# Optimization experiments

Hardware: AMD Instinct MI355X
Metric: run time of the kernel (lower is better)

The kernel has to match this reference:

```python
import jax, jax.numpy as jnp
import numpy as np

NU, EU = 40000, 640000          # user-graph nodes / edges
B, T, NW, ET = 64, 16, 30, 60    # users, tweets/user, words/tweet, edges/tweet
NT = B * T * NW                  # 30720 tweet word-nodes
NTE = B * T * ET                 # 61440 tweet edges
NSEG_T = B * T                   # 1024 tweet segments


def gcn_conv(x, src, dst, W, b, N):
    """PyG GCNConv: x@W, add self loops, sym deg-normalize, scatter-add, +b."""
    x = x @ W
    loop = jnp.arange(N)
    s = jnp.concatenate([src, loop])
    d = jnp.concatenate([dst, loop])
    deg = jax.ops.segment_sum(jnp.ones_like(d, dtype=x.dtype), d, num_segments=N)
    dinv = jnp.where(deg > 0, jax.lax.rsqrt(deg), 0.0)
    norm = dinv[s] * dinv[d]                     # [E+N]
    out = jax.ops.segment_sum(x[s] * norm[:, None], d, num_segments=N)
    return out + b


def att_pool(x, seg, nseg, W1, b1, W2, b2):
    """AttentionalAggregation: gate_nn = Linear->Linear, segment softmax, weighted sum."""
    gate = (x @ W1 + b1) @ W2 + b2               # [N, C]
    m = jax.ops.segment_max(gate, seg, num_segments=nseg)
    e = jnp.exp(gate - m[seg])
    s = jax.ops.segment_sum(e, seg, num_segments=nseg)
    a = e / (s[seg] + 1e-16)
    return jax.ops.segment_sum(a * x, seg, num_segments=nseg)  # [nseg, C]


def gru_last(x_seq, W_ih, W_hh, b_ih, b_hh):
    """torch.nn.GRU, 1 layer; x_seq [B,T,C] -> final hidden [B,C]."""
    C = W_hh.shape[1]
    h0 = jnp.zeros((x_seq.shape[0], C), x_seq.dtype)
    def step(h, x):
        gi = x @ W_ih.T + b_ih
        gh = h @ W_hh.T + b_hh
        ir, iz, inn = jnp.split(gi, 3, axis=-1)
        hr, hz, hn = jnp.split(gh, 3, axis=-1)
        r = jax.nn.sigmoid(ir + hr)
        z = jax.nn.sigmoid(iz + hz)
        n = jnp.tanh(inn + r * hn)
        return (1.0 - z) * n + z * h, None
    hT, _ = jax.lax.scan(step, h0, jnp.swapaxes(x_seq, 0, 1))
    return hT


def setup_inputs():
    ks = jax.random.split(jax.random.key(0), 24)
    def rn(i, shape, s=1.0):
        return jax.random.normal(ks[i], shape, dtype=jnp.float32) * s
    z = lambda n_: jnp.zeros((n_,), jnp.float32)
    inp = {}
    inp["user_x"] = rn(0, (NU, 128))
    inp["user_feats"] = rn(1, (B, 32))
    inp["tweet_x"] = rn(2, (NT, 768))
    inp["Wu0"] = rn(3, (128, 128), 0.1); inp["bu0"] = z(128)
    inp["Wu1"] = rn(4, (128, 128), 0.1); inp["bu1"] = z(128)
    inp["Wgu1"] = rn(5, (128, 128), 0.1); inp["bgu1"] = z(128)
    inp["Wgu2"] = rn(6, (128, 128), 0.1); inp["bgu2"] = z(128)
    inp["Wt0"] = rn(7, (768, 256), 0.05); inp["bt0"] = z(256)
    inp["Wt1"] = rn(8, (256, 128), 0.1); inp["bt1"] = z(128)
    inp["Wgt1"] = rn(9, (128, 128), 0.1); inp["bgt1"] = z(128)
    inp["Wgt2"] = rn(10, (128, 128), 0.1); inp["bgt2"] = z(128)
    inp["W_ih"] = rn(11, (384, 128), 0.1); inp["b_ih"] = z(384)
    inp["W_hh"] = rn(12, (384, 128), 0.1); inp["b_hh"] = z(384)
    inp["Wd0"] = rn(13, (288, 256), 0.1); inp["bd0"] = z(256)
    inp["Wd1"] = rn(14, (256, 64), 0.1); inp["bd1"] = z(64)
    inp["Wp"] = rn(15, (64, 1), 0.1); inp["bp"] = z(1)
    inp["user_edge_index"] = jax.random.randint(ks[16], (2, EU), 0, NU)
    local = jax.random.randint(ks[17], (2, NTE), 0, NW)
    offs = jnp.repeat(jnp.arange(NSEG_T) * NW, ET)   # edges stay inside each tweet
    inp["tweet_edge_index"] = local + offs[None, :]
    inp["user_batch"] = jnp.arange(NU) // (NU // B)  # contiguous per-user segments (ptr)
    inp["tweet_batch"] = jnp.arange(NT) // NW        # contiguous per-tweet segments (ptr)
    return inp


def reference(user_x, user_feats, tweet_x,
              Wu0, bu0, Wu1, bu1, Wgu1, bgu1, Wgu2, bgu2,
              Wt0, bt0, Wt1, bt1, Wgt1, bgt1, Wgt2, bgt2,
              W_ih, b_ih, W_hh, b_hh,
              Wd0, bd0, Wd1, bd1, Wp, bp,
              user_edge_index, tweet_edge_index, user_batch, tweet_batch):
    h = jax.nn.relu(gcn_conv(user_x, user_edge_index[0], user_edge_index[1], Wu0, bu0, NU))
    h = jax.nn.relu(gcn_conv(h, user_edge_index[0], user_edge_index[1], Wu1, bu1, NU))
    user_pool = att_pool(h, user_batch, B, Wgu1, bgu1, Wgu2, bgu2)        # [B,128]
    g = jax.nn.relu(gcn_conv(tweet_x, tweet_edge_index[0], tweet_edge_index[1], Wt0, bt0, NT))
    g = jax.nn.relu(gcn_conv(g, tweet_edge_index[0], tweet_edge_index[1], Wt1, bt1, NT))
    tweet_pool = att_pool(g, tweet_batch, NSEG_T, Wgt1, bgt1, Wgt2, bgt2)  # [B*T,128]
    tweet_seq = tweet_pool.reshape(B, T, 128)
    tweet_h = gru_last(tweet_seq, W_ih, W_hh, b_ih, b_hh)                 # [B,128]
    # head
    full = jnp.concatenate([user_feats, user_pool, tweet_h], axis=1)      # [B,288]
    full = jax.nn.relu(full @ Wd0 + bd0)
    full = jax.nn.relu(full @ Wd1 + bd1)
    return jax.nn.sigmoid(full @ Wp + bp)                                 # [B,1]
```

## Files before the change

kernel.cpp:

```cpp
#include <hip/hip_runtime.h>
#include <hip/hip_bf16.h>

#define NU 40000
#define EU 640000
#define BB 64
#define TT 16
#define NW 30
#define NTNODES 30720
#define NTE 61440
#define NSEG_T 1024
#define NCHUNK 16
#define NBU 157
#define NBT 120

typedef __attribute__((ext_vector_type(8))) short bf16x8;
typedef __attribute__((ext_vector_type(4))) float f32x4;

__device__ __forceinline__ unsigned short f2bf(float x) {
    union { float f; unsigned u; } v; v.f = x;
    unsigned r = v.u + 0x7FFFu + ((v.u >> 16) & 1u);
    return (unsigned short)(r >> 16);
}
__device__ __forceinline__ float bf2f(unsigned short u) {
    union { unsigned u; float f; } v; v.u = (unsigned)u << 16; return v.f;
}
__device__ __forceinline__ void gld16(const unsigned short* g, unsigned short* l) {
    __builtin_amdgcn_global_load_lds(
        (const __attribute__((address_space(1))) void*)g,
        (__attribute__((address_space(3))) void*)l, 16, 0, 0);
}

__global__ void k_zeroint(int* __restrict__ p, int n) {
    int i = blockIdx.x * blockDim.x + threadIdx.x;
    if (i < n) p[i] = 0;
}

__global__ void k_hist2(const int* __restrict__ ue_dst, const int* __restrict__ te_dst,
                        int* __restrict__ hist_u, int* __restrict__ hist_t) {
    int i = blockIdx.x * blockDim.x + threadIdx.x;
    if (i < EU) atomicAdd(&hist_u[ue_dst[i]], 1);
    else if (i < EU + NTE) atomicAdd(&hist_t[te_dst[i - EU]], 1);
}

__global__ __launch_bounds__(256) void k_scan_a2(const int* __restrict__ hist_u,
                                                 int* __restrict__ bsum_u,
                                                 int* __restrict__ bsum_t) {
    __shared__ int red[256];
    int b = blockIdx.x, t = threadIdx.x;
    const int* h; int* bs; int n, lb;
    if (b < NBU) { h = hist_u;      bs = bsum_u; n = NU;      lb = b; }
    else         { h = hist_u + NU; bs = bsum_t; n = NTNODES; lb = b - NBU; }
    int i = lb * 256 + t;
    red[t] = (i < n) ? h[i] : 0;
    __syncthreads();
    for (int off = 128; off; off >>= 1) {
        if (t < off) red[t] += red[t + off];
        __syncthreads();
    }
    if (t == 0) bs[lb] = red[0];
}

__global__ __launch_bounds__(256) void k_scan_b2(int* __restrict__ bsum_u,
                                                 int* __restrict__ bsum_t) {
    __shared__ int s[256];
    int t = threadIdx.x;
    int* bs = blockIdx.x ? bsum_t : bsum_u;
    int nb  = blockIdx.x ? NBT : NBU;
    s[t] = (t < nb) ? bs[t] : 0;
    __syncthreads();
    for (int off = 1; off < 256; off <<= 1) {
        int v = (t >= off) ? s[t - off] : 0;
        __syncthreads();
        s[t] += v;
        __syncthreads();
    }
    if (t < nb) bs[t] = (t == 0) ? 0 : s[t - 1];
}

__global__ __launch_bounds__(256) void k_scan_c2(const int* __restrict__ hist_u,
                                                 const int* __restrict__ bsum_u,
                                                 const int* __restrict__ bsum_t,
                                                 int* __restrict__ ptr_u, int* __restrict__ fill_u,
                                                 int* __restrict__ ptr_t, int* __restrict__ fill_t,
                                                 float* __restrict__ dinv_u) {
    __shared__ int s[256];
    int b = blockIdx.x, t = threadIdx.x;
    const int *h, *bs; int *ptr, *fill; int n, lb; float* dv;
    if (b < NBU) { h = hist_u;      bs = bsum_u; ptr = ptr_u; fill = fill_u; n = NU;      lb = b;       dv = dinv_u; }
    else         { h = hist_u + NU; bs = bsum_t; ptr = ptr_t; fill = fill_t; n = NTNODES; lb = b - NBU; dv = dinv_u + NU; }
    int i = lb * 256 + t;
    int hv = (i < n) ? h[i] : 0;
    s[t] = hv;
    __syncthreads();
    for (int off = 1; off < 256; off <<= 1) {
        int v = (t >= off) ? s[t - off] : 0;
        __syncthreads();
        s[t] += v;
        __syncthreads();
    }
    if (i < n) {
        int excl = bs[lb] + s[t] - hv;
        ptr[i] = excl;
        fill[i] = excl;
        dv[i] = rsqrtf((float)hv + 1.0f);
        if (i == n - 1) ptr[n] = excl + hv;
    }
}

__global__ void k_place2(const int* __restrict__ ue_src, const int* __restrict__ ue_dst,
                         const int* __restrict__ te_src, const int* __restrict__ te_dst,
                         int* __restrict__ fill_u, int* __restrict__ esrc_u,
                         int* __restrict__ fill_t, int* __restrict__ esrc_t) {
    int e = blockIdx.x * blockDim.x + threadIdx.x;
    if (e < EU) {
        int pos = atomicAdd(&fill_u[ue_dst[e]], 1);
        esrc_u[pos] = ue_src[e];
    } else if (e < EU + NTE) {
        int e2 = e - EU;
        int pos = atomicAdd(&fill_t[te_dst[e2]], 1);
        esrc_t[pos] = te_src[e2];
    }
}

__global__ void k_transpose(const float* __restrict__ in, float* __restrict__ out,
                            int R, int K) {
    int idx = blockIdx.x * blockDim.x + threadIdx.x;
    if (idx >= R * K) return;
    int j = idx / K, k = idx - j * K;
    out[k * R + j] = in[idx];
}

__device__ __forceinline__ void pack_one(const float* __restrict__ W,
                                         unsigned short* __restrict__ out,
                                         int f, int K, int N, int trans) {
    int j = f & 7;
    int chunk = f >> 3;
    int c = chunk & 511;
    int panel = chunk >> 9;
    int KS = K >> 5;
    int ks = panel % KS;
    int bn = panel / KS;
    int n = bn * 128 + (c & 127);
    int k = ks * 32 + (c >> 7) * 8 + j;
    float v = trans ? W[(size_t)n * K + k] : W[(size_t)k * N + n];
    out[f] = f2bf(v);
}

__global__ void k_packall(const float* __restrict__ Wu0, const float* __restrict__ Wu1,
                          const float* __restrict__ Wgu1, const float* __restrict__ Wgu2,
                          const float* __restrict__ Wt0, const float* __restrict__ Wt1,
                          const float* __restrict__ Wgt1, const float* __restrict__ Wgt2,
                          const float* __restrict__ Wih,
                          unsigned short* __restrict__ pk) {
    int f = blockIdx.x * blockDim.x + threadIdx.x;
    if (f < 16384)        pack_one(Wu0,  pk + 0,      f,          128, 128, 0);
    else if (f < 32768)   pack_one(Wu1,  pk + 16384,  f - 16384,  128, 128, 0);
    else if (f < 49152)   pack_one(Wgu1, pk + 32768,  f - 32768,  128, 128, 0);
    else if (f < 65536)   pack_one(Wgu2, pk + 49152,  f - 49152,  128, 128, 0);
    else if (f < 262144)  pack_one(Wt0,  pk + 65536,  f - 65536,  768, 256, 0);
    else if (f < 294912)  pack_one(Wt1,  pk + 262144, f - 262144, 256, 128, 0);
    else if (f < 311296)  pack_one(Wgt1, pk + 294912, f - 294912, 128, 128, 0);
    else if (f < 327680)  pack_one(Wgt2, pk + 311296, f - 311296, 128, 128, 0);
    else if (f < 376832)  pack_one(Wih,  pk + 327680, f - 327680, 128, 384, 1);
}

template<bool AF32>
__global__ __launch_bounds__(256) void k_mgemm(const void* __restrict__ Araw,
                                               const unsigned short* __restrict__ Bpk,
                                               const float* __restrict__ bias,
                                               void* __restrict__ Craw,
                                               int M, int K, int N, int flags) {
    constexpr int AST = AF32 ? 260 : 256;
    __shared__ unsigned short Alds[8 * AST];
    __shared__ unsigned short Blds[8192];
    int tid = threadIdx.x, lane = tid & 63, w = tid >> 6;
    int bm = blockIdx.x, bn = blockIdx.y;
    int wr = (w >> 1) * 16, wc = (w & 1) * 64;
    int l15 = lane & 15, lk = lane >> 4;

    f32x4 acc[4];
#pragma unroll
    for (int n = 0; n < 4; ++n) acc[n] = (f32x4){0.f, 0.f, 0.f, 0.f};

    const unsigned short* Bpanel = Bpk + (size_t)bn * (K >> 5) * 4096;
    int KS64 = K >> 6;

    for (int ks = 0; ks < KS64; ++ks) {
        int k0 = ks * 64;
        {
            const unsigned short* bg = Bpanel + (size_t)ks * 8192;
#pragma unroll
            for (int q = 0; q < 4; ++q) {
                int off = (w * 4 + q) * 512;
                gld16(bg + off + lane * 8, &Blds[off]);
            }
        }
        if (AF32) {
            const float* A = (const float*)Araw;
#pragma unroll
            for (int p = 0; p < 2; ++p) {
                int f4 = p * 256 + tid;
                int row = f4 >> 4;
                int kq  = f4 & 15;
                float4 av = *(const float4*)(A + (size_t)(bm * 32 + row) * K + k0 + kq * 4);
                unsigned lo = (unsigned)f2bf(av.x) | ((unsigned)f2bf(av.y) << 16);
                unsigned hi = (unsigned)f2bf(av.z) | ((unsigned)f2bf(av.w) << 16);
                int off = (kq >> 1) * AST + row * 8 + (kq & 1) * 4;
                *(uint2*)&Alds[off] = make_uint2(lo, hi);
            }
        } else {
            const unsigned short* A = (const unsigned short*)Araw;
            int kblk = 2 * w + (lane >> 5);
            int row = lane & 31;
            gld16(A + (size_t)(bm * 32 + row) * K + k0 + kblk * 8,
                  &Alds[w * 512]);
        }
        __syncthreads();
#pragma unroll
        for (int h = 0; h < 2; ++h) {
            int kb = h * 4 + lk;
            bf16x8 a = *(const bf16x8*)&Alds[kb * AST + (wr + l15) * 8];
            bf16x8 b[4];
#pragma unroll
            for (int n = 0; n < 4; ++n)
                b[n] = *(const bf16x8*)&Blds[kb * 1024 + (wc + n * 16 + l15) * 8];
#pragma unroll
            for (int n = 0; n < 4; ++n)
                acc[n] = __builtin_amdgcn_mfma_f32_16x16x32_bf16(a, b[n], acc[n], 0, 0, 0);
        }
        __syncthreads();
    }

    int grow0 = bm * 32 + wr + lk * 4;
#pragma unroll
    for (int n = 0; n < 4; ++n) {
        int gcol = bn * 128 + wc + n * 16 + l15;
        float bv = (flags & 1) ? bias[gcol] : 0.f;
#pragma unroll
        for (int i = 0; i < 4; ++i) {
            int grow = grow0 + i;
            float v = acc[n][i] + bv;
            if (flags & 2) v = fmaxf(v, 0.f);
            if (flags & 4) ((float*)Craw)[(size_t)grow * N + gcol] = v;
            else ((unsigned short*)Craw)[(size_t)grow * N + gcol] = f2bf(v);
        }
    }
}

__global__ __launch_bounds__(256) void k_gatepair(const unsigned short* __restrict__ X,
                                                  const unsigned short* __restrict__ W1,
                                                  const float* __restrict__ b1,
                                                  const unsigned short* __restrict__ W2,
                                                  const float* __restrict__ b2,
                                                  unsigned short* __restrict__ outp, int M) {
    __shared__ unsigned short Ax[16 * 512];
    __shared__ unsigned short Wl[8192];
    int tid = threadIdx.x, lane = tid & 63, w = tid >> 6;
    int bm = blockIdx.x;
    int wr = (w >> 1) * 32, wc = (w & 1) * 64;
    int l15 = lane & 15, lk = lane >> 4;

#pragma unroll
    for (int q = 0; q < 4; ++q) {
        int pl = w * 4 + q;
        gld16(X + (size_t)(bm * 64 + lane) * 128 + pl * 8, &Ax[pl * 512]);
    }

    f32x4 acc[2][4];
#pragma unroll
    for (int m = 0; m < 2; ++m)
#pragma unroll
        for (int n = 0; n < 4; ++n) acc[m][n] = (f32x4){0.f, 0.f, 0.f, 0.f};

    for (int ks = 0; ks < 2; ++ks) {
        const unsigned short* wp = W1 + ks * 8192;
#pragma unroll
        for (int q = 0; q < 4; ++q) {
            int off = (w * 4 + q) * 512;
            gld16(wp + off + lane * 8, &Wl[off]);
        }
        __syncthreads();
#pragma unroll
        for (int h = 0; h < 2; ++h) {
            int kb = h * 4 + lk;
            bf16x8 a[2], b[4];
#pragma unroll
            for (int m = 0; m < 2; ++m)
                a[m] = *(const bf16x8*)&Ax[(ks * 8 + kb) * 512 + (wr + m * 16 + l15) * 8];
#pragma unroll
            for (int n = 0; n < 4; ++n)
                b[n] = *(const bf16x8*)&Wl[kb * 1024 + (wc + n * 16 + l15) * 8];
#pragma unroll
            for (int m = 0; m < 2; ++m)
#pragma unroll
                for (int n = 0; n < 4; ++n)
                    acc[m][n] = __builtin_amdgcn_mfma_f32_16x16x32_bf16(a[m], b[n], acc[m][n], 0, 0, 0);
        }
        __syncthreads();
    }

#pragma unroll
    for (int m = 0; m < 2; ++m)
#pragma unroll
        for (int n = 0; n < 4; ++n) {
            int col = wc + n * 16 + l15;
            float bv = b1[col];
#pragma unroll
            for (int i = 0; i < 4; ++i) {
                int row = wr + m * 16 + lk * 4 + i;
                float v = acc[m][n][i] + bv;
                Ax[(col >> 3) * 512 + row * 8 + (col & 7)] = f2bf(v);
            }
        }
    __syncthreads();

#pragma unroll
    for (int m = 0; m < 2; ++m)
#pragma unroll
        for (int n = 0; n < 4; ++n) acc[m][n] = (f32x4){0.f, 0.f, 0.f, 0.f};
    for (int ks = 0; ks < 2; ++ks) {
        const unsigned short* wp = W2 + ks * 8192;
#pragma unroll
        for (int q = 0; q < 4; ++q) {
            int off = (w * 4 + q) * 512;
            gld16(wp + off + lane * 8, &Wl[off]);
        }
        __syncthreads();
#pragma unroll
        for (int h = 0; h < 2; ++h) {
            int kb = h * 4 + lk;
            bf16x8 a[2], b[4];
#pragma unroll
            for (int m = 0; m < 2; ++m)
                a[m] = *(const bf16x8*)&Ax[(ks * 8 + kb) * 512 + (wr + m * 16 + l15) * 8];
#pragma unroll
            for (int n = 0; n < 4; ++n)
                b[n] = *(const bf16x8*)&Wl[kb * 1024 + (wc + n * 16 + l15) * 8];
#pragma unroll
            for (int m = 0; m < 2; ++m)
#pragma unroll
                for (int n = 0; n < 4; ++n)
                    acc[m][n] = __builtin_amdgcn_mfma_f32_16x16x32_bf16(a[m], b[n], acc[m][n], 0, 0, 0);
        }
        __syncthreads();
    }

#pragma unroll
    for (int m = 0; m < 2; ++m)
#pragma unroll
        for (int n = 0; n < 4; ++n) {
            int col = wc + n * 16 + l15;
            float bv = b2[col];
#pragma unroll
            for (int i = 0; i < 4; ++i) {
                int row = bm * 64 + wr + m * 16 + lk * 4 + i;
                float v = acc[m][n][i] + bv;
                outp[(size_t)row * 128 + col] = f2bf(v);
            }
        }
}

__global__ __launch_bounds__(256) void k_gagg(const unsigned short* __restrict__ y,
                                              const int* __restrict__ ptr,
                                              const int* __restrict__ esrc,
                                              const float* __restrict__ dinv,
                                              const float* __restrict__ bias,
                                              unsigned short* __restrict__ ob, int N, int nch) {
    int idx = blockIdx.x * 4 + (threadIdx.x >> 6);
    if (idx >= N * nch) return;
    int v = idx / nch, ch = idx - v * nch;
    int C = nch << 7;
    int lane = threadIdx.x & 63;
    int c0 = (ch << 7) + lane * 2;
    float dv = dinv[v];
    unsigned yv = *(const unsigned*)(y + (size_t)v * C + c0);
    float a0 = dv * dv * bf2f((unsigned short)yv);
    float a1 = dv * dv * bf2f((unsigned short)(yv >> 16));
    int e = ptr[v], e1 = ptr[v + 1];
    for (; e + 3 < e1; e += 4) {
        int s0 = esrc[e], s1 = esrc[e + 1], s2 = esrc[e + 2], s3 = esrc[e + 3];
        float cc0 = dv * dinv[s0], cc1 = dv * dinv[s1];
        float cc2 = dv * dinv[s2], cc3 = dv * dinv[s3];
        unsigned w0 = *(const unsigned*)(y + (size_t)s0 * C + c0);
        unsigned w1 = *(const unsigned*)(y + (size_t)s1 * C + c0);
        unsigned w2 = *(const unsigned*)(y + (size_t)s2 * C + c0);
        unsigned w3 = *(const unsigned*)(y + (size_t)s3 * C + c0);
        a0 += cc0 * bf2f((unsigned short)w0) + cc1 * bf2f((unsigned short)w1)
            + cc2 * bf2f((unsigned short)w2) + cc3 * bf2f((unsigned short)w3);
        a1 += cc0 * bf2f((unsigned short)(w0 >> 16)) + cc1 * bf2f((unsigned short)(w1 >> 16))
            + cc2 * bf2f((unsigned short)(w2 >> 16)) + cc3 * bf2f((unsigned short)(w3 >> 16));
    }
    for (; e < e1; ++e) {
        int s0 = esrc[e];
        float cc0 = dv * dinv[s0];
        unsigned w0 = *(const unsigned*)(y + (size_t)s0 * C + c0);
        a0 += cc0 * bf2f((unsigned short)w0);
        a1 += cc0 * bf2f((unsigned short)(w0 >> 16));
    }
    a0 = fmaxf(a0 + bias[c0], 0.f);
    a1 = fmaxf(a1 + bias[c0 + 1], 0.f);
    *(unsigned*)(ob + (size_t)v * C + c0) = (unsigned)f2bf(a0) | ((unsigned)f2bf(a1) << 16);
}

__global__ __launch_bounds__(128) void k_attpool(const unsigned short* __restrict__ x,
                                                 const unsigned short* __restrict__ gate,
                                                 unsigned short* __restrict__ outb, int S) {
    int seg = blockIdx.x;
    int c = threadIdx.x;
    size_t base = (size_t)seg * S * 128 + c;
    float m = -1e30f;
    for (int n = 0; n < S; ++n) m = fmaxf(m, bf2f(gate[base + (size_t)n * 128]));
    float se = 0.f, acc = 0.f;
    for (int n = 0; n < S; ++n) {
        float g = bf2f(gate[base + (size_t)n * 128]);
        float e = expf(g - m);
        se += e;
        acc += e * bf2f(x[base + (size_t)n * 128]);
    }
    outb[(size_t)seg * 128 + c] = f2bf(acc / (se + 1e-16f));
}

__global__ __launch_bounds__(256) void k_pool_pmax(const unsigned short* __restrict__ gate,
                                                   float* __restrict__ pmax, int S) {
    int seg = blockIdx.x, ch = blockIdx.y;
    int c = threadIdx.x & 127, j = threadIdx.x >> 7;
    int csz = (S + NCHUNK - 1) / NCHUNK;
    int n0 = ch * csz, n1 = min(S, n0 + csz);
    size_t base = (size_t)seg * S * 128 + c;
    float m = -1e30f;
    for (int n = n0 + j; n < n1; n += 2)
        m = fmaxf(m, bf2f(gate[base + (size_t)n * 128]));
    __shared__ float red[2][128];
    red[j][c] = m;
    __syncthreads();
    if (j == 0)
        pmax[((size_t)seg * NCHUNK + ch) * 128 + c] = fmaxf(red[0][c], red[1][c]);
}

__global__ __launch_bounds__(256) void k_pool_psum(const unsigned short* __restrict__ x,
                                                   const unsigned short* __restrict__ gate,
                                                   const float* __restrict__ pmax,
                                                   float* __restrict__ pse,
                                                   float* __restrict__ pacc, int S) {
    int seg = blockIdx.x, ch = blockIdx.y;
    int c = threadIdx.x & 127, j = threadIdx.x >> 7;
    int csz = (S + NCHUNK - 1) / NCHUNK;
    int n0 = ch * csz, n1 = min(S, n0 + csz);
    size_t base = (size_t)seg * S * 128 + c;
    float m = -1e30f;
#pragma unroll
    for (int ch2 = 0; ch2 < NCHUNK; ++ch2)
        m = fmaxf(m, pmax[((size_t)seg * NCHUNK + ch2) * 128 + c]);
    float se = 0.f, acc = 0.f;
    for (int n = n0 + j; n < n1; n += 2) {
        float g = bf2f(gate[base + (size_t)n * 128]);
        float e = expf(g - m);
        se += e;
        acc += e * bf2f(x[base + (size_t)n * 128]);
    }
    __shared__ float rs[2][128], ra[2][128];
    rs[j][c] = se; ra[j][c] = acc;
    __syncthreads();
    if (j == 0) {
        size_t o = ((size_t)seg * NCHUNK + ch) * 128 + c;
        pse[o]  = rs[0][c] + rs[1][c];
        pacc[o] = ra[0][c] + ra[1][c];
    }
}

__global__ __launch_bounds__(128) void k_pool_final(const float* __restrict__ pse,
                                                    const float* __restrict__ pacc,
                                                    float* __restrict__ out) {
    int seg = blockIdx.x, c = threadIdx.x;
    float se = 0.f, acc = 0.f;
    for (int ch = 0; ch < NCHUNK; ++ch) {
        size_t o = ((size_t)seg * NCHUNK + ch) * 128 + c;
        se += pse[o];
        acc += pacc[o];
    }
    out[(size_t)seg * 128 + c] = acc / (se + 1e-16f);
}

__global__ __launch_bounds__(768) void k_gru_rec(const float* __restrict__ gi,
                                                 const float* __restrict__ whhT,
                                                 const float* __restrict__ bhh,
                                                 float* __restrict__ hT) {
    __shared__ float hs[128];
    __shared__ float ph[768];
    int b = blockIdx.x, t = threadIdx.x;
    int half = (t >= 384) ? 1 : 0;
    int j = t - half * 384;
    float w[64];
#pragma unroll
    for (int i = 0; i < 64; ++i)
        w[i] = whhT[(half * 64 + i) * 384 + j];
    float chr = 0.f, chz = 0.f, chn = 0.f;
    if (t < 128) {
        hs[t] = 0.f;
        chr = bhh[t]; chz = bhh[128 + t]; chn = bhh[256 + t];
    }
    __syncthreads();
    for (int step = 0; step < TT; ++step) {
        float a0 = 0.f, a1 = 0.f, a2 = 0.f, a3 = 0.f;
        const float* hbase = hs + half * 64;
#pragma unroll
        for (int i = 0; i < 64; i += 4) {
            float4 hv = *(const float4*)(hbase + i);
            a0 += hv.x * w[i + 0];
            a1 += hv.y * w[i + 1];
            a2 += hv.z * w[i + 2];
            a3 += hv.w * w[i + 3];
        }
        ph[t] = (a0 + a1) + (a2 + a3);
        __syncthreads();
        float hnew = 0.f;
        if (t < 128) {
            const float* girow = gi + ((size_t)b * TT + step) * 384;
            float hr = ph[t] + ph[t + 384] + chr;
            float hz = ph[128 + t] + ph[512 + t] + chz;
            float hn = ph[256 + t] + ph[640 + t] + chn;
            float ir = girow[t], iz = girow[128 + t], in = girow[256 + t];
            float r = 1.f / (1.f + expf(-(ir + hr)));
            float z = 1.f / (1.f + expf(-(iz + hz)));
            float n = tanhf(in + r * hn);
            hnew = (1.f - z) * n + z * hs[t];
        }
        __syncthreads();
        if (t < 128) hs[t] = hnew;
        __syncthreads();
    }
    if (t < 128) hT[(size_t)b * 128 + t] = hs[t];
}

__global__ __launch_bounds__(256) void k_head(const float* __restrict__ uf,
                                              const float* __restrict__ up,
                                              const float* __restrict__ th,
                                              const float* __restrict__ Wd0, const float* __restrict__ bd0,
                                              const float* __restrict__ Wd1, const float* __restrict__ bd1,
                                              const float* __restrict__ Wp, const float* __restrict__ bp,
                                              float* __restrict__ out) {
    __shared__ float in0[288], l1[256], l2[64];
    int b = blockIdx.x, t = threadIdx.x;
    if (t < 32) in0[t] = uf[b * 32 + t];
    else if (t < 160) in0[t] = up[b * 128 + (t - 32)];
    if (t < 128) in0[160 + t] = th[b * 128 + t];
    __syncthreads();
    float acc = bd0[t];
    for (int k = 0; k < 288; ++k) acc += in0[k] * Wd0[k * 256 + t];
    l1[t] = fmaxf(acc, 0.f);
    __syncthreads();
    if (t < 64) {
        float a2 = bd1[t];
        for (int k = 0; k < 256; ++k) a2 += l1[k] * Wd1[k * 64 + t];
        l2[t] = fmaxf(a2, 0.f);
    }
    __syncthreads();
    if (t < 64) {
        float p = l2[t] * Wp[t];
        for (int off = 32; off; off >>= 1) p += __shfl_down(p, off, 64);
        if (t == 0) out[b] = 1.f / (1.f + expf(-(p + bp[0])));
    }
}

extern "C" void kernel_launch(void* const* d_in, const int* in_sizes, int n_in,
                              void* d_out, int out_size, void* d_ws, size_t ws_size,
                              hipStream_t stream) {
    const float* user_x     = (const float*)d_in[0];
    const float* user_feats = (const float*)d_in[1];
    const float* tweet_x    = (const float*)d_in[2];
    const float* Wu0 = (const float*)d_in[3];  const float* bu0 = (const float*)d_in[4];
    const float* Wu1 = (const float*)d_in[5];  const float* bu1 = (const float*)d_in[6];
    const float* Wgu1 = (const float*)d_in[7]; const float* bgu1 = (const float*)d_in[8];
    const float* Wgu2 = (const float*)d_in[9]; const float* bgu2 = (const float*)d_in[10];
    const float* Wt0 = (const float*)d_in[11]; const float* bt0 = (const float*)d_in[12];
    const float* Wt1 = (const float*)d_in[13]; const float* bt1 = (const float*)d_in[14];
    const float* Wgt1 = (const float*)d_in[15]; const float* bgt1 = (const float*)d_in[16];
    const float* Wgt2 = (const float*)d_in[17]; const float* bgt2 = (const float*)d_in[18];
    const float* W_ih = (const float*)d_in[19]; const float* b_ih = (const float*)d_in[20];
    const float* W_hh = (const float*)d_in[21]; const float* b_hh = (const float*)d_in[22];
    const float* Wd0 = (const float*)d_in[23]; const float* bd0 = (const float*)d_in[24];
    const float* Wd1 = (const float*)d_in[25]; const float* bd1 = (const float*)d_in[26];
    const float* Wp  = (const float*)d_in[27]; const float* bp  = (const float*)d_in[28];
    const int* ue = (const int*)d_in[29];
    const int* te = (const int*)d_in[30];
    const int* ue_src = ue, *ue_dst = ue + EU;
    const int* te_src = te, *te_dst = te + NTE;

    float* ws = (float*)d_ws;
    size_t o = 0;
    float* dinv_u = ws + o;     o += NU;
    float* dinv_t = ws + o;     o += NTNODES;
    float* user_pool = ws + o;  o += (size_t)BB * 128;
    float* tweet_h = ws + o;    o += (size_t)BB * 128;
    float* whhT = ws + o;       o += 128 * 384;
    float* gi = ws + o;         o += (size_t)NSEG_T * 384;
    float* pmax = ws + o;       o += 131072;
    float* pse = ws + o;        o += 131072;
    float* pacc = ws + o;       o += 131072;
    int* iw = (int*)(ws + o);
    int* hist_u = iw;
    int* hist_t = iw + NU;
    int* ptr_u  = iw + NU + NTNODES;
    int* fill_u = ptr_u + NU + 1;
    int* esrc_u = fill_u + NU;
    int* ptr_t  = esrc_u + EU;
    int* fill_t = ptr_t + NTNODES + 1;
    int* esrc_t = fill_t + NTNODES;
    int* bsum_u = esrc_t + NTE;
    int* bsum_t = bsum_u + 256;
    unsigned short* pk = (unsigned short*)(((uintptr_t)(bsum_t + 256) + 15) & ~(uintptr_t)15);
    unsigned short* pWu0  = pk;
    unsigned short* pWu1  = pWu0  + 16384;
    unsigned short* pWgu1 = pWu1  + 16384;
    unsigned short* pWgu2 = pWgu1 + 16384;
    unsigned short* pWt0  = pWgu2 + 16384;
    unsigned short* pWt1  = pWt0  + 196608;
    unsigned short* pWgt1 = pWt1  + 32768;
    unsigned short* pWgt2 = pWgt1 + 16384;
    unsigned short* pWih  = pWgt2 + 16384;
    unsigned short* arena = (unsigned short*)(((uintptr_t)(pWih + 49152) + 15) & ~(uintptr_t)15);
    const size_t SLOT = (size_t)NTNODES * 256;
    unsigned short* P0 = arena;
    unsigned short* P1 = P0 + SLOT;
    unsigned short* P2 = P1 + SLOT;
    unsigned short* P3 = P2 + SLOT;
    unsigned short* tpool_bf = P3 + SLOT;
    float* out = (float*)d_out;

    dim3 b256(256);
    const int GMU = NU / 32;
    const int GMT = NTNODES / 32;
    const float* NB = nullptr;

    hipLaunchKernelGGL(k_packall, dim3((376832 + 255) / 256), b256, 0, stream,
                       Wu0, Wu1, Wgu1, Wgu2, Wt0, Wt1, Wgt1, Wgt2, W_ih, pk);
    hipLaunchKernelGGL(k_transpose, dim3((384 * 128 + 255) / 256), b256, 0, stream,
                       W_hh, whhT, 384, 128);

    hipLaunchKernelGGL(k_zeroint, dim3((NU + NTNODES + 255) / 256), b256, 0, stream,
                       hist_u, NU + NTNODES);
    hipLaunchKernelGGL(k_hist2, dim3((EU + NTE + 255) / 256), b256, 0, stream,
                       ue_dst, te_dst, hist_u, hist_t);
    hipLaunchKernelGGL(k_scan_a2, dim3(NBU + NBT), b256, 0, stream, hist_u, bsum_u, bsum_t);
    hipLaunchKernelGGL(k_scan_b2, dim3(2), b256, 0, stream, bsum_u, bsum_t);
    hipLaunchKernelGGL(k_scan_c2, dim3(NBU + NBT), b256, 0, stream,
                       hist_u, bsum_u, bsum_t, ptr_u, fill_u, ptr_t, fill_t, dinv_u);
    hipLaunchKernelGGL(k_place2, dim3((EU + NTE + 255) / 256), b256, 0, stream,
                       ue_src, ue_dst, te_src, te_dst, fill_u, esrc_u, fill_t, esrc_t);

    hipLaunchKernelGGL(HIP_KERNEL_NAME(k_mgemm<true>), dim3(GMT, 2), b256, 0, stream,
                       (const void*)tweet_x, pWt0, NB, (void*)P0, NTNODES, 768, 256, 0);
    hipLaunchKernelGGL(k_gagg, dim3((NTNODES * 2 + 3) / 4), b256, 0, stream,
                       P0, ptr_t, esrc_t, dinv_t, bt0, P1, NTNODES, 2);

    hipLaunchKernelGGL(HIP_KERNEL_NAME(k_mgemm<true>), dim3(GMU, 1), b256, 0, stream,
                       (const void*)user_x, pWu0, NB, (void*)P3, NU, 128, 128, 0);
    hipLaunchKernelGGL(k_gagg, dim3((NU + 3) / 4), b256, 0, stream,
                       P3, ptr_u, esrc_u, dinv_u, bu0, P0, NU, 1);
    hipLaunchKernelGGL(HIP_KERNEL_NAME(k_mgemm<false>), dim3(GMU, 1), b256, 0, stream,
                       (const void*)P0, pWu1, NB, (void*)P2, NU, 128, 128, 0);
    hipLaunchKernelGGL(k_gagg, dim3((NU + 3) / 4), b256, 0, stream,
                       P2, ptr_u, esrc_u, dinv_u, bu1, P3, NU, 1);
    hipLaunchKernelGGL(k_gatepair, dim3(NU / 64), b256, 0, stream,
                       P3, pWgu1, bgu1, pWgu2, bgu2, P0, NU);
    hipLaunchKernelGGL(k_pool_pmax, dim3(BB, NCHUNK), b256, 0, stream, P0, pmax, NU / BB);
    hipLaunchKernelGGL(k_pool_psum, dim3(BB, NCHUNK), b256, 0, stream,
                       P3, P0, pmax, pse, pacc, NU / BB);
    hipLaunchKernelGGL(k_pool_final, dim3(BB), dim3(128), 0, stream, pse, pacc, user_pool);

    hipLaunchKernelGGL(HIP_KERNEL_NAME(k_mgemm<false>), dim3(GMT, 1), b256, 0, stream,
                       (const void*)P1, pWt1, NB, (void*)P2, NTNODES, 256, 128, 0);
    hipLaunchKernelGGL(k_gagg, dim3((NTNODES + 3) / 4), b256, 0, stream,
                       P2, ptr_t, esrc_t, dinv_t, bt1, P3, NTNODES, 1);
    hipLaunchKernelGGL(k_gatepair, dim3(NTNODES / 64), b256, 0, stream,
                       P3, pWgt1, bgt1, pWgt2, bgt2, P1, NTNODES);
    hipLaunchKernelGGL(k_attpool, dim3(NSEG_T), dim3(128), 0, stream,
                       P3, P1, tpool_bf, NW);

    hipLaunchKernelGGL(HIP_KERNEL_NAME(k_mgemm<false>), dim3(NSEG_T / 32, 3), b256, 0, stream,
                       (const void*)tpool_bf, pWih, b_ih, (void*)gi, NSEG_T, 128, 384, 5);
    hipLaunchKernelGGL(k_gru_rec, dim3(BB), dim3(768), 0, stream,
                       gi, whhT, b_hh, tweet_h);

    hipLaunchKernelGGL(k_head, dim3(BB), b256, 0, stream,
                       user_feats, user_pool, tweet_h,
                       Wd0, bd0, Wd1, bd1, Wp, bp, out);
}
```

Measured before the change: 345.1 us.

## Use 128x128 MFMA GEMM tiles and pre-convert fp32 inputs to bf16

Replaces the 32-row GEMM tile with a 128x128 tile where each wave computes a 64x64 block using a 4x4 grid of MFMA accumulators. This raises operand reuse per LDS load and cuts redundant B-panel reads across blocks. A separate conversion kernel now casts user_x and tweet_x to bf16 up front, so every GEMM takes bf16 inputs through async global-to-LDS loads. In exchange, the conversion adds an extra full pass over the large tweet_x input plus a write of its bf16 copy, and the larger tiles yield far fewer blocks for the small GEMMs (for example, 8 blocks on the 1024-row input-projection GEMM).

```diff
diff --git a/kernel.cpp b/kernel.cpp
--- a/kernel.cpp
+++ b/kernel.cpp
@@ -128,6 +128,25 @@
     if (idx >= R * K) return;
     int j = idx / K, k = idx - j * K;
     out[k * R + j] = in[idx];
+}
+
+#define NUX ((long)NU * 128)
+#define NTX ((long)NTNODES * 768)
+__global__ void k_cvt2(const float* __restrict__ ux, const float* __restrict__ tx,
+                       unsigned short* __restrict__ xu, unsigned short* __restrict__ xt) {
+    long i = ((long)blockIdx.x * blockDim.x + threadIdx.x) * 8;
+    const float* src; unsigned short* dst; long j;
+    if (i < NUX) { src = ux; dst = xu; j = i; }
+    else if (i < NUX + NTX) { src = tx; dst = xt; j = i - NUX; }
+    else return;
+    float4 a = *(const float4*)(src + j);
+    float4 b = *(const float4*)(src + j + 4);
+    uint4 r;
+    r.x = (unsigned)f2bf(a.x) | ((unsigned)f2bf(a.y) << 16);
+    r.y = (unsigned)f2bf(a.z) | ((unsigned)f2bf(a.w) << 16);
+    r.z = (unsigned)f2bf(b.x) | ((unsigned)f2bf(b.y) << 16);
+    r.w = (unsigned)f2bf(b.z) | ((unsigned)f2bf(b.w) << 16);
+    *(uint4*)(dst + j) = r;
 }
 
 __device__ __forceinline__ void pack_one(const float* __restrict__ W,
@@ -164,85 +183,79 @@
     else if (f < 376832)  pack_one(Wih,  pk + 327680, f - 327680, 128, 384, 1);
 }
 
-template<bool AF32>
-__global__ __launch_bounds__(256) void k_mgemm(const void* __restrict__ Araw,
-                                               const unsigned short* __restrict__ Bpk,
-                                               const float* __restrict__ bias,
-                                               void* __restrict__ Craw,
-                                               int M, int K, int N, int flags) {
-    constexpr int AST = AF32 ? 260 : 256;
-    __shared__ unsigned short Alds[8 * AST];
-    __shared__ unsigned short Blds[8192];
+__global__ __launch_bounds__(256) void k_mgemm128(const unsigned short* __restrict__ A,
+                                                  const unsigned short* __restrict__ Bpk,
+                                                  const float* __restrict__ bias,
+                                                  void* __restrict__ Craw,
+                                                  int M, int K, int N, int flags) {
+    __shared__ unsigned short Alds[4096];
+    __shared__ unsigned short Blds[4096];
     int tid = threadIdx.x, lane = tid & 63, w = tid >> 6;
     int bm = blockIdx.x, bn = blockIdx.y;
-    int wr = (w >> 1) * 16, wc = (w & 1) * 64;
+    int wr = (w >> 1) * 64, wc = (w & 1) * 64;
     int l15 = lane & 15, lk = lane >> 4;
 
-    f32x4 acc[4];
-#pragma unroll
-    for (int n = 0; n < 4; ++n) acc[n] = (f32x4){0.f, 0.f, 0.f, 0.f};
-
-    const unsigned short* Bpanel = Bpk + (size_t)bn * (K >> 5) * 4096;
-    int KS64 = K >> 6;
-
-    for (int ks = 0; ks < KS64; ++ks) {
-        int k0 = ks * 64;
+    f32x4 acc[4][4];
+#pragma unroll
+    for (int m = 0; m < 4; ++m)
+#pragma unroll
+        for (int n = 0; n < 4; ++n) acc[m][n] = (f32x4){0.f, 0.f, 0.f, 0.f};
+
+    int KS = K >> 5;
+    const unsigned short* Bpanel = Bpk + (size_t)bn * KS * 4096;
+
+    for (int ks = 0; ks < KS; ++ks) {
+        int k0 = ks * 32;
         {
-            const unsigned short* bg = Bpanel + (size_t)ks * 8192;
-#pragma unroll
-            for (int q = 0; q < 4; ++q) {
-                int off = (w * 4 + q) * 512;
-                gld16(bg + off + lane * 8, &Blds[off]);
+            const unsigned short* bg = Bpanel + (size_t)ks * 4096;
+#pragma unroll
+            for (int q = 0; q < 2; ++q) {
+                int i = w * 2 + q;
+                gld16(bg + i * 512 + lane * 8, &Blds[i * 512]);
             }
         }
-        if (AF32) {
-            const float* A = (const float*)Araw;
-#pragma unroll
-            for (int p = 0; p < 2; ++p) {
-                int f4 = p * 256 + tid;
-                int row = f4 >> 4;
-                int kq  = f4 & 15;
-                float4 av = *(const float4*)(A + (size_t)(bm * 32 + row) * K + k0 + kq * 4);
-                unsigned lo = (unsigned)f2bf(av.x) | ((unsigned)f2bf(av.y) << 16);
-                unsigned hi = (unsigned)f2bf(av.z) | ((unsigned)f2bf(av.w) << 16);
-                int off = (kq >> 1) * AST + row * 8 + (kq & 1) * 4;
-                *(uint2*)&Alds[off] = make_uint2(lo, hi);
+#pragma unroll
+        for (int q = 0; q < 2; ++q) {
+            int i = w * 2 + q;
+            int kblk = i >> 1, half = i & 1;
+            int rg = bm * 128 + half * 64 + lane;
+            rg = rg < M ? rg : M - 1;
+            gld16(A + (size_t)rg * K + k0 + kblk * 8,
+                  &Alds[kblk * 1024 + half * 512]);
+        }
+        __syncthreads();
+        bf16x8 a[4], b[4];
+#pragma unroll
+        for (int m = 0; m < 4; ++m)
+            a[m] = *(const bf16x8*)&Alds[lk * 1024 + (wr + m * 16 + l15) * 8];
+#pragma unroll
+        for (int n = 0; n < 4; ++n)
+            b[n] = *(const bf16x8*)&Blds[lk * 1024 + (wc + n * 16 + l15) * 8];
+#pragma unroll
+        for (int m = 0; m < 4; ++m)
+#pragma unroll
+            for (int n = 0; n < 4; ++n)
+                acc[m][n] = __builtin_amdgcn_mfma_f32_16x16x32_bf16(a[m], b[n], acc[m][n], 0, 0, 0);
+        __syncthreads();
+    }
+
+#pragma unroll
+    for (int m = 0; m < 4; ++m) {
+        int grow0 = bm * 128 + wr + m * 16 + lk * 4;
+#pragma unroll
+        for (int n = 0; n < 4; ++n) {
+            int gcol = bn * 128 + wc + n * 16 + l15;
+            float bv = (flags & 1) ? bias[gcol] : 0.f;
+#pragma unroll
+            for (int i = 0; i < 4; ++i) {
+                int grow = grow0 + i;
+                if (grow < M) {
+                    float v = acc[m][n][i] + bv;
+                    if (flags & 2) v = fmaxf(v, 0.f);
+                    if (flags & 4) ((float*)Craw)[(size_t)grow * N + gcol] = v;
+                    else ((unsigned short*)Craw)[(size_t)grow * N + gcol] = f2bf(v);
+                }
             }
-        } else {
-            const unsigned short* A = (const unsigned short*)Araw;
-            int kblk = 2 * w + (lane >> 5);
-            int row = lane & 31;
-            gld16(A + (size_t)(bm * 32 + row) * K + k0 + kblk * 8,
-                  &Alds[w * 512]);
-        }
-        __syncthreads();
-#pragma unroll
-        for (int h = 0; h < 2; ++h) {
-            int kb = h * 4 + lk;
-            bf16x8 a = *(const bf16x8*)&Alds[kb * AST + (wr + l15) * 8];
-            bf16x8 b[4];
-#pragma unroll
-            for (int n = 0; n < 4; ++n)
-                b[n] = *(const bf16x8*)&Blds[kb * 1024 + (wc + n * 16 + l15) * 8];
-#pragma unroll
-            for (int n = 0; n < 4; ++n)
-                acc[n] = __builtin_amdgcn_mfma_f32_16x16x32_bf16(a, b[n], acc[n], 0, 0, 0);
-        }
-        __syncthreads();
-    }
-
-    int grow0 = bm * 32 + wr + lk * 4;
-#pragma unroll
-    for (int n = 0; n < 4; ++n) {
-        int gcol = bn * 128 + wc + n * 16 + l15;
-        float bv = (flags & 1) ? bias[gcol] : 0.f;
-#pragma unroll
-        for (int i = 0; i < 4; ++i) {
-            int grow = grow0 + i;
-            float v = acc[n][i] + bv;
-            if (flags & 2) v = fmaxf(v, 0.f);
-            if (flags & 4) ((float*)Craw)[(size_t)grow * N + gcol] = v;
-            else ((unsigned short*)Craw)[(size_t)grow * N + gcol] = f2bf(v);
         }
     }
 }
@@ -625,17 +638,21 @@
     unsigned short* P2 = P1 + SLOT;
     unsigned short* P3 = P2 + SLOT;
     unsigned short* tpool_bf = P3 + SLOT;
+    unsigned short* xt = P1;
+    unsigned short* xu = tpool_bf + 131072;
     float* out = (float*)d_out;
 
     dim3 b256(256);
-    const int GMU = NU / 32;
-    const int GMT = NTNODES / 32;
+    const int GMU = (NU + 127) / 128;
+    const int GMT = NTNODES / 128;
     const float* NB = nullptr;
 
     hipLaunchKernelGGL(k_packall, dim3((376832 + 255) / 256), b256, 0, stream,
                        Wu0, Wu1, Wgu1, Wgu2, Wt0, Wt1, Wgt1, Wgt2, W_ih, pk);
     hipLaunchKernelGGL(k_transpose, dim3((384 * 128 + 255) / 256), b256, 0, stream,
                        W_hh, whhT, 384, 128);
+    hipLaunchKernelGGL(k_cvt2, dim3((int)((NUX + NTX) / 8 / 256 + 1)), b256, 0, stream,
+                       user_x, tweet_x, xu, xt);
 
     hipLaunchKernelGGL(k_zeroint, dim3((NU + NTNODES + 255) / 256), b256, 0, stream,
                        hist_u, NU + NTNODES);
@@ -648,17 +665,17 @@
     hipLaunchKernelGGL(k_place2, dim3((EU + NTE + 255) / 256), b256, 0, stream,
                        ue_src, ue_dst, te_src, te_dst, fill_u, esrc_u, fill_t, esrc_t);
 
-    hipLaunchKernelGGL(HIP_KERNEL_NAME(k_mgemm<true>), dim3(GMT, 2), b256, 0, stream,
-                       (const void*)tweet_x, pWt0, NB, (void*)P0, NTNODES, 768, 256, 0);
+    hipLaunchKernelGGL(k_mgemm128, dim3(GMT, 2), b256, 0, stream,
+                       xt, pWt0, NB, (void*)P0, NTNODES, 768, 256, 0);
     hipLaunchKernelGGL(k_gagg, dim3((NTNODES * 2 + 3) / 4), b256, 0, stream,
                        P0, ptr_t, esrc_t, dinv_t, bt0, P1, NTNODES, 2);
 
-    hipLaunchKernelGGL(HIP_KERNEL_NAME(k_mgemm<true>), dim3(GMU, 1), b256, 0, stream,
-                       (const void*)user_x, pWu0, NB, (void*)P3, NU, 128, 128, 0);
+    hipLaunchKernelGGL(k_mgemm128, dim3(GMU, 1), b256, 0, stream,
+                       xu, pWu0, NB, (void*)P3, NU, 128, 128, 0);
     hipLaunchKernelGGL(k_gagg, dim3((NU + 3) / 4), b256, 0, stream,
                        P3, ptr_u, esrc_u, dinv_u, bu0, P0, NU, 1);
-    hipLaunchKernelGGL(HIP_KERNEL_NAME(k_mgemm<false>), dim3(GMU, 1), b256, 0, stream,
-                       (const void*)P0, pWu1, NB, (void*)P2, NU, 128, 128, 0);
+    hipLaunchKernelGGL(k_mgemm128, dim3(GMU, 1), b256, 0, stream,
+                       P0, pWu1, NB, (void*)P2, NU, 128, 128, 0);
     hipLaunchKernelGGL(k_gagg, dim3((NU + 3) / 4), b256, 0, stream,
                        P2, ptr_u, esrc_u, dinv_u, bu1, P3, NU, 1);
     hipLaunchKernelGGL(k_gatepair, dim3(NU / 64), b256, 0, stream,
@@ -668,8 +685,8 @@
                        P3, P0, pmax, pse, pacc, NU / BB);
     hipLaunchKernelGGL(k_pool_final, dim3(BB), dim3(128), 0, stream, pse, pacc, user_pool);
 
-    hipLaunchKernelGGL(HIP_KERNEL_NAME(k_mgemm<false>), dim3(GMT, 1), b256, 0, stream,
-                       (const void*)P1, pWt1, NB, (void*)P2, NTNODES, 256, 128, 0);
+    hipLaunchKernelGGL(k_mgemm128, dim3(GMT, 1), b256, 0, stream,
+                       P1, pWt1, NB, (void*)P2, NTNODES, 256, 128, 0);
     hipLaunchKernelGGL(k_gagg, dim3((NTNODES + 3) / 4), b256, 0, stream,
                        P2, ptr_t, esrc_t, dinv_t, bt1, P3, NTNODES, 1);
     hipLaunchKernelGGL(k_gatepair, dim3(NTNODES / 64), b256, 0, stream,
@@ -677,8 +694,8 @@
     hipLaunchKernelGGL(k_attpool, dim3(NSEG_T), dim3(128), 0, stream,
                        P3, P1, tpool_bf, NW);
 
-    hipLaunchKernelGGL(HIP_KERNEL_NAME(k_mgemm<false>), dim3(NSEG_T / 32, 3), b256, 0, stream,
-                       (const void*)tpool_bf, pWih, b_ih, (void*)gi, NSEG_T, 128, 384, 5);
+    hipLaunchKernelGGL(k_mgemm128, dim3(NSEG_T / 128, 3), b256, 0, stream,
+                       tpool_bf, pWih, b_ih, (void*)gi, NSEG_T, 128, 384, 5);
     hipLaunchKernelGGL(k_gru_rec, dim3(BB), dim3(768), 0, stream,
                        gi, whhT, b_hh, tweet_h);
 
```

Result: slower. 410.9 us (+19.1%).

## Fold GCN source-side degree scaling into GEMM epilogue and merge transpose into pack

Applied to the files above, without the earlier changes.

Each GCN layer's feature GEMM now scales its output rows by dinv, so the aggregation kernel sums neighbor rows without gathering dinv per edge, applying the destination dinv once at the end. This removes per-edge dinv loads and multiplies from the gather-heavy aggregation. The W_hh transpose is folded into the weight-packing kernel, saving one launch. Rows are scaled before bf16 rounding, which slightly changes numerics.

```diff
diff --git a/kernel.cpp b/kernel.cpp
--- a/kernel.cpp
+++ b/kernel.cpp
@@ -122,14 +122,6 @@
     }
 }
 
-__global__ void k_transpose(const float* __restrict__ in, float* __restrict__ out,
-                            int R, int K) {
-    int idx = blockIdx.x * blockDim.x + threadIdx.x;
-    if (idx >= R * K) return;
-    int j = idx / K, k = idx - j * K;
-    out[k * R + j] = in[idx];
-}
-
 __device__ __forceinline__ void pack_one(const float* __restrict__ W,
                                          unsigned short* __restrict__ out,
                                          int f, int K, int N, int trans) {
@@ -151,6 +143,7 @@
                           const float* __restrict__ Wt0, const float* __restrict__ Wt1,
                           const float* __restrict__ Wgt1, const float* __restrict__ Wgt2,
                           const float* __restrict__ Wih,
+                          const float* __restrict__ Whh, float* __restrict__ whhT,
                           unsigned short* __restrict__ pk) {
     int f = blockIdx.x * blockDim.x + threadIdx.x;
     if (f < 16384)        pack_one(Wu0,  pk + 0,      f,          128, 128, 0);
@@ -162,12 +155,18 @@
     else if (f < 311296)  pack_one(Wgt1, pk + 294912, f - 294912, 128, 128, 0);
     else if (f < 327680)  pack_one(Wgt2, pk + 311296, f - 311296, 128, 128, 0);
     else if (f < 376832)  pack_one(Wih,  pk + 327680, f - 327680, 128, 384, 1);
+    else if (f < 425984) {
+        int j2 = f - 376832;
+        int r = j2 >> 7, k2 = j2 & 127;
+        whhT[k2 * 384 + r] = Whh[j2];
+    }
 }
 
 template<bool AF32>
 __global__ __launch_bounds__(256) void k_mgemm(const void* __restrict__ Araw,
                                                const unsigned short* __restrict__ Bpk,
                                                const float* __restrict__ bias,
+                                               const float* __restrict__ dscale,
                                                void* __restrict__ Craw,
                                                int M, int K, int N, int flags) {
     constexpr int AST = AF32 ? 260 : 256;
@@ -233,13 +232,14 @@
 
     int grow0 = bm * 32 + wr + lk * 4;
 #pragma unroll
-    for (int n = 0; n < 4; ++n) {
-        int gcol = bn * 128 + wc + n * 16 + l15;
-        float bv = (flags & 1) ? bias[gcol] : 0.f;
-#pragma unroll
-        for (int i = 0; i < 4; ++i) {
-            int grow = grow0 + i;
-            float v = acc[n][i] + bv;
+    for (int i = 0; i < 4; ++i) {
+        int grow = grow0 + i;
+        float ds = dscale ? dscale[grow] : 1.f;
+#pragma unroll
+        for (int n = 0; n < 4; ++n) {
+            int gcol = bn * 128 + wc + n * 16 + l15;
+            float v = acc[n][i] * ds;
+            if (flags & 1) v += bias[gcol];
             if (flags & 2) v = fmaxf(v, 0.f);
             if (flags & 4) ((float*)Craw)[(size_t)grow * N + gcol] = v;
             else ((unsigned short*)Craw)[(size_t)grow * N + gcol] = f2bf(v);
@@ -372,33 +372,30 @@
     int C = nch << 7;
     int lane = threadIdx.x & 63;
     int c0 = (ch << 7) + lane * 2;
-    float dv = dinv[v];
     unsigned yv = *(const unsigned*)(y + (size_t)v * C + c0);
-    float a0 = dv * dv * bf2f((unsigned short)yv);
-    float a1 = dv * dv * bf2f((unsigned short)(yv >> 16));
+    float a0 = bf2f((unsigned short)yv);
+    float a1 = bf2f((unsigned short)(yv >> 16));
     int e = ptr[v], e1 = ptr[v + 1];
     for (; e + 3 < e1; e += 4) {
         int s0 = esrc[e], s1 = esrc[e + 1], s2 = esrc[e + 2], s3 = esrc[e + 3];
-        float cc0 = dv * dinv[s0], cc1 = dv * dinv[s1];
-        float cc2 = dv * dinv[s2], cc3 = dv * dinv[s3];
         unsigned w0 = *(const unsigned*)(y + (size_t)s0 * C + c0);
         unsigned w1 = *(const unsigned*)(y + (size_t)s1 * C + c0);
         unsigned w2 = *(const unsigned*)(y + (size_t)s2 * C + c0);
         unsigned w3 = *(const unsigned*)(y + (size_t)s3 * C + c0);
-        a0 += cc0 * bf2f((unsigned short)w0) + cc1 * bf2f((unsigned short)w1)
-            + cc2 * bf2f((unsigned short)w2) + cc3 * bf2f((unsigned short)w3);
-        a1 += cc0 * bf2f((unsigned short)(w0 >> 16)) + cc1 * bf2f((unsigned short)(w1 >> 16))
-            + cc2 * bf2f((unsigned short)(w2 >> 16)) + cc3 * bf2f((unsigned short)(w3 >> 16));
+        a0 += bf2f((unsigned short)w0) + bf2f((unsigned short)w1)
+            + bf2f((unsigned short)w2) + bf2f((unsigned short)w3);
+        a1 += bf2f((unsigned short)(w0 >> 16)) + bf2f((unsigned short)(w1 >> 16))
+            + bf2f((unsigned short)(w2 >> 16)) + bf2f((unsigned short)(w3 >> 16));
     }
     for (; e < e1; ++e) {
         int s0 = esrc[e];
-        float cc0 = dv * dinv[s0];
         unsigned w0 = *(const unsigned*)(y + (size_t)s0 * C + c0);
-        a0 += cc0 * bf2f((unsigned short)w0);
-        a1 += cc0 * bf2f((unsigned short)(w0 >> 16));
-    }
-    a0 = fmaxf(a0 + bias[c0], 0.f);
-    a1 = fmaxf(a1 + bias[c0 + 1], 0.f);
+        a0 += bf2f((unsigned short)w0);
+        a1 += bf2f((unsigned short)(w0 >> 16));
+    }
+    float dv = dinv[v];
+    a0 = fmaxf(dv * a0 + bias[c0], 0.f);
+    a1 = fmaxf(dv * a1 + bias[c0 + 1], 0.f);
     *(unsigned*)(ob + (size_t)v * C + c0) = (unsigned)f2bf(a0) | ((unsigned)f2bf(a1) << 16);
 }
 
@@ -631,11 +628,10 @@
     const int GMU = NU / 32;
     const int GMT = NTNODES / 32;
     const float* NB = nullptr;
-
-    hipLaunchKernelGGL(k_packall, dim3((376832 + 255) / 256), b256, 0, stream,
-                       Wu0, Wu1, Wgu1, Wgu2, Wt0, Wt1, Wgt1, Wgt2, W_ih, pk);
-    hipLaunchKernelGGL(k_transpose, dim3((384 * 128 + 255) / 256), b256, 0, stream,
-                       W_hh, whhT, 384, 128);
+    const float* ND = nullptr;
+
+    hipLaunchKernelGGL(k_packall, dim3((425984 + 255) / 256), b256, 0, stream,
+                       Wu0, Wu1, Wgu1, Wgu2, Wt0, Wt1, Wgt1, Wgt2, W_ih, W_hh, whhT, pk);
 
     hipLaunchKernelGGL(k_zeroint, dim3((NU + NTNODES + 255) / 256), b256, 0, stream,
                        hist_u, NU + NTNODES);
@@ -649,16 +645,16 @@
                        ue_src, ue_dst, te_src, te_dst, fill_u, esrc_u, fill_t, esrc_t);
 
     hipLaunchKernelGGL(HIP_KERNEL_NAME(k_mgemm<true>), dim3(GMT, 2), b256, 0, stream,
-                       (const void*)tweet_x, pWt0, NB, (void*)P0, NTNODES, 768, 256, 0);
+                       (const void*)tweet_x, pWt0, NB, dinv_t, (void*)P0, NTNODES, 768, 256, 0);
     hipLaunchKernelGGL(k_gagg, dim3((NTNODES * 2 + 3) / 4), b256, 0, stream,
                        P0, ptr_t, esrc_t, dinv_t, bt0, P1, NTNODES, 2);
 
     hipLaunchKernelGGL(HIP_KERNEL_NAME(k_mgemm<true>), dim3(GMU, 1), b256, 0, stream,
-                       (const void*)user_x, pWu0, NB, (void*)P3, NU, 128, 128, 0);
+                       (const void*)user_x, pWu0, NB, dinv_u, (void*)P3, NU, 128, 128, 0);
     hipLaunchKernelGGL(k_gagg, dim3((NU + 3) / 4), b256, 0, stream,
                        P3, ptr_u, esrc_u, dinv_u, bu0, P0, NU, 1);
     hipLaunchKernelGGL(HIP_KERNEL_NAME(k_mgemm<false>), dim3(GMU, 1), b256, 0, stream,
-                       (const void*)P0, pWu1, NB, (void*)P2, NU, 128, 128, 0);
+                       (const void*)P0, pWu1, NB, dinv_u, (void*)P2, NU, 128, 128, 0);
     hipLaunchKernelGGL(k_gagg, dim3((NU + 3) / 4), b256, 0, stream,
                        P2, ptr_u, esrc_u, dinv_u, bu1, P3, NU, 1);
     hipLaunchKernelGGL(k_gatepair, dim3(NU / 64), b256, 0, stream,
@@ -669,7 +665,7 @@
     hipLaunchKernelGGL(k_pool_final, dim3(BB), dim3(128), 0, stream, pse, pacc, user_pool);
 
     hipLaunchKernelGGL(HIP_KERNEL_NAME(k_mgemm<false>), dim3(GMT, 1), b256, 0, stream,
-                       (const void*)P1, pWt1, NB, (void*)P2, NTNODES, 256, 128, 0);
+                       (const void*)P1, pWt1, NB, dinv_t, (void*)P2, NTNODES, 256, 128, 0);
     hipLaunchKernelGGL(k_gagg, dim3((NTNODES + 3) / 4), b256, 0, stream,
                        P2, ptr_t, esrc_t, dinv_t, bt1, P3, NTNODES, 1);
     hipLaunchKernelGGL(k_gatepair, dim3(NTNODES / 64), b256, 0, stream,
@@ -678,7 +674,7 @@
                        P3, P1, tpool_bf, NW);
 
     hipLaunchKernelGGL(HIP_KERNEL_NAME(k_mgemm<false>), dim3(NSEG_T / 32, 3), b256, 0, stream,
-                       (const void*)tpool_bf, pWih, b_ih, (void*)gi, NSEG_T, 128, 384, 5);
+                       (const void*)tpool_bf, pWih, b_ih, ND, (void*)gi, NSEG_T, 128, 384, 5);
     hipLaunchKernelGGL(k_gru_rec, dim3(BB), dim3(768), 0, stream,
                        gi, whhT, b_hh, tweet_h);
 
```

Measured after the change: 347.5 us. About the same (+0.7%).
